# Performance work log

Measured on AMD Instinct MI355X. Metric: run time of the kernel, lower is better.

The kernel has to match this reference:

```python
import jax, jax.numpy as jnp
import numpy as np

B, S, D = 4, 2048, 1024
H = 16
HD = D // H  # 64
BASE = 10000.0


def _rope_cache(seq_len, dim):
    inv_freq = 1.0 / (BASE ** (jnp.arange(0, dim, 2, dtype=jnp.float32) / dim))
    t = jnp.arange(seq_len, dtype=jnp.float32)
    freqs = jnp.einsum('i,j->ij', t, inv_freq)          # [S, dim/2]
    emb = jnp.concatenate([freqs, freqs], axis=-1)      # [S, dim]
    return jnp.cos(emb), jnp.sin(emb)


def _rotate_half(x):
    x1, x2 = jnp.split(x, 2, axis=-1)
    return jnp.concatenate([-x2, x1], axis=-1)


def setup_inputs() -> dict:
    key = jax.random.key(0)
    ks = jax.random.split(key, 5)
    scale = 1.0 / np.sqrt(D)
    return {
        'x': jax.random.normal(ks[0], (B, S, D), dtype=jnp.float32),
        'Wq': jax.random.normal(ks[1], (D, D), dtype=jnp.float32) * scale,
        'Wk': jax.random.normal(ks[2], (D, D), dtype=jnp.float32) * scale,
        'Wv': jax.random.normal(ks[3], (D, D), dtype=jnp.float32) * scale,
        'Wo': jax.random.normal(ks[4], (D, D), dtype=jnp.float32) * scale,
    }


def reference(x, Wq, Wk, Wv, Wo):
    b, s, d = x.shape
    # projections (torch Linear, no bias): y = x @ W.T
    q = (x @ Wq.T).reshape(b, s, H, HD).transpose(0, 2, 1, 3)  # [B,H,S,HD]
    k = (x @ Wk.T).reshape(b, s, H, HD).transpose(0, 2, 1, 3)
    v = (x @ Wv.T).reshape(b, s, H, HD).transpose(0, 2, 1, 3)
    cos, sin = _rope_cache(s, HD)  # [S, HD]
    cos = cos[None, None]
    sin = sin[None, None]
    q = q * cos + _rotate_half(q) * sin
    k = k * cos + _rotate_half(k) * sin
    scale = 1.0 / np.sqrt(HD)
    attn = jnp.einsum('bhqd,bhkd->bhqk', q, k) * scale  # [B,H,S,S]
    attn = jax.nn.softmax(attn, axis=-1)
    out = jnp.einsum('bhqk,bhkd->bhqd', attn, v)
    out = out.transpose(0, 2, 1, 3).reshape(b, s, d)
    return out @ Wo.T
```

## Files before the change

### kernel.cpp

```cpp
#include <hip/hip_runtime.h>
#include <math.h>
#include <stdint.h>

#define BB 4
#define SS 2048
#define DDIM 1024
#define HH 16
#define HD 64
#define QKVLD 3072
#define QSCALE (0.125f * 1.44269504089f)

typedef __bf16 bf16x8 __attribute__((ext_vector_type(8)));
typedef float f32x4 __attribute__((ext_vector_type(4)));
typedef float f32x16 __attribute__((ext_vector_type(16)));
typedef int i32x4 __attribute__((ext_vector_type(4)));

__device__ __forceinline__ unsigned short f2bf(float f) {
    union { float f; unsigned u; } v; v.f = f;
    unsigned r = (v.u + 0x7FFFu + ((v.u >> 16) & 1u)) >> 16;
    return (unsigned short)r;
}
__device__ __forceinline__ void gload_lds16(const unsigned short* g, unsigned char* s) {
    __builtin_amdgcn_global_load_lds(
        (const __attribute__((address_space(1))) unsigned int*)(g),
        (__attribute__((address_space(3))) unsigned int*)(s), 16, 0, 0);
}

__global__ void prep_all(const float* __restrict__ x,
                         const float* __restrict__ Wq, const float* __restrict__ Wk,
                         const float* __restrict__ Wv, const float* __restrict__ Wo,
                         unsigned short* __restrict__ xb,
                         unsigned short* __restrict__ wqkv, unsigned short* __restrict__ wob,
                         float* __restrict__ cosT, float* __restrict__ sinT) {
    int bid = blockIdx.x;
    if (bid < 8192) {
        int i = bid * 256 + threadIdx.x;
        float4 v = ((const float4*)x)[i];
        ushort4 o;
        o.x = f2bf(v.x); o.y = f2bf(v.y); o.z = f2bf(v.z); o.w = f2bf(v.w);
        ((ushort4*)xb)[i] = o;
    } else if (bid < 12288) {
        int i = (bid - 8192) * 256 + threadIdx.x;
        int mat = i >> 18;
        int off = i & 262143;
        const float* src = (mat == 0) ? Wq : (mat == 1) ? Wk : (mat == 2) ? Wv : Wo;
        unsigned short* dst = (mat < 3) ? (wqkv + (size_t)mat * 1048576) : wob;
        float4 v = ((const float4*)src)[off];
        ushort4 o;
        o.x = f2bf(v.x); o.y = f2bf(v.y); o.z = f2bf(v.z); o.w = f2bf(v.w);
        ((ushort4*)dst)[off] = o;
    } else {
        int idx = (bid - 12288) * 256 + threadIdx.x;
        int s = idx >> 5;
        int j = idx & 31;
        float invf = powf(10000.0f, -(float)j / 32.0f);
        float ang = (float)s * invf;
        cosT[idx] = cosf(ang);
        sinT[idx] = sinf(ang);
    }
}

__global__ __launch_bounds__(512) void gemm256_qkv(const unsigned short* __restrict__ A,
                                                   const unsigned short* __restrict__ Bm,
                                                   unsigned short* __restrict__ C,
                                                   const float* __restrict__ cosT,
                                                   const float* __restrict__ sinT,
                                                   unsigned short* __restrict__ vt) {
    __shared__ unsigned char smem[131072];
    const int t = threadIdx.x;
    const int l = t & 63;
    const int w = t >> 6;
    const int wm = w >> 2;
    const int wn = w & 3;
    const int K = DDIM;
    const int NT = K >> 6;

    const int bid = blockIdx.y * gridDim.x + blockIdx.x;
    const int cpx = (gridDim.x * gridDim.y) >> 3;
    const int swz = (bid & 7) * cpx + (bid >> 3);
    const int row0 = (swz / gridDim.x) * 256;
    const int col0 = (swz % gridDim.x) * 256;

    f32x4 acc[8][4];
#pragma unroll
    for (int i = 0; i < 8; ++i)
#pragma unroll
        for (int j = 0; j < 4; ++j) acc[i][j] = f32x4{0.f, 0.f, 0.f, 0.f};

    const unsigned short* aSg = A + (size_t)(row0 + w * 16 + (l >> 3)) * K + ((l & 7) ^ (l >> 3)) * 8;
    const unsigned short* bSg = Bm + (size_t)(col0 + w * 16 + (l >> 3)) * K + ((l & 7) ^ (l >> 3)) * 8;
    const int dRow = (w * 16) * 128;

#define STAGE_A(kt, h, j, buf) \
    gload_lds16(aSg + (size_t)((h) * 128 + (j) * 8) * K + (kt) * 64, \
                smem + (buf) * 65536 + (h) * 16384 + dRow + (j) * 1024)
#define STAGE_B(kt, h, j, buf) \
    gload_lds16(bSg + (size_t)((h) * 128 + (j) * 8) * K + (kt) * 64, \
                smem + (buf) * 65536 + 32768 + (h) * 16384 + dRow + (j) * 1024)

    STAGE_B(0, 0, 0, 0); STAGE_B(0, 0, 1, 0); STAGE_B(0, 1, 0, 0); STAGE_B(0, 1, 1, 0);
    STAGE_A(0, 0, 0, 0); STAGE_A(0, 0, 1, 0); STAGE_A(0, 1, 0, 0); STAGE_A(0, 1, 1, 0);
    STAGE_B(1, 0, 0, 1); STAGE_B(1, 0, 1, 1); STAGE_B(1, 1, 0, 1); STAGE_B(1, 1, 1, 1);
    asm volatile("s_waitcnt vmcnt(4)" ::: "memory");
    __builtin_amdgcn_s_barrier();

    const int cA = (l >> 4) << 4;
    const int swr = (l & 7) << 4;
    const int rA0 = wm * 128 + (l & 15);
    const int rB0 = wn * 64 + (l & 15);

    int cur = 0;
    for (int u = 0; u < NT; ++u) {
        const int nxt = cur ^ 1;
        const unsigned char* Ab = smem + cur * 65536;
        const unsigned char* Bb = smem + cur * 65536 + 32768;
        const bool pA = (u + 1 < NT);
        const bool pB = (u + 2 < NT);
        bf16x8 bfr[4][2];

#pragma unroll
        for (int p = 0; p < 4; ++p) {
            if (p == 0) { if (pA) { STAGE_A(u + 1, 0, 0, nxt); STAGE_A(u + 1, 0, 1, nxt); } }
            if (p == 1) { if (pA) { STAGE_A(u + 1, 1, 0, nxt); STAGE_A(u + 1, 1, 1, nxt); } }
            if (p == 2) { if (pB) { STAGE_B(u + 2, 0, 0, cur); STAGE_B(u + 2, 0, 1, cur); } }
            if (p == 3) { if (pB) { STAGE_B(u + 2, 1, 0, cur); STAGE_B(u + 2, 1, 1, cur); } }

            if (p == 0) {
#pragma unroll
                for (int ni = 0; ni < 4; ++ni)
#pragma unroll
                    for (int kk = 0; kk < 2; ++kk) {
                        int row = rB0 + ni * 16;
                        bfr[ni][kk] = *(const bf16x8*)(Bb + (row * 128 + ((kk * 64 + cA) ^ swr)));
                    }
            }
            bf16x8 af[2][2];
#pragma unroll
            for (int m2 = 0; m2 < 2; ++m2)
#pragma unroll
                for (int kk = 0; kk < 2; ++kk) {
                    int row = rA0 + (p * 2 + m2) * 16;
                    af[m2][kk] = *(const bf16x8*)(Ab + (row * 128 + ((kk * 64 + cA) ^ swr)));
                }

            __builtin_amdgcn_s_barrier();
            asm volatile("s_waitcnt lgkmcnt(0)" ::: "memory");
            __builtin_amdgcn_sched_barrier(0);
            __builtin_amdgcn_s_setprio(1);
#pragma unroll
            for (int m2 = 0; m2 < 2; ++m2)
#pragma unroll
                for (int ni = 0; ni < 4; ++ni)
#pragma unroll
                    for (int kk = 0; kk < 2; ++kk)
                        acc[p * 2 + m2][ni] = __builtin_amdgcn_mfma_f32_16x16x32_bf16(
                            af[m2][kk], bfr[ni][kk], acc[p * 2 + m2][ni], 0, 0, 0);
            __builtin_amdgcn_s_setprio(0);
            if (p == 3) {
                if (u < NT - 2) asm volatile("s_waitcnt vmcnt(4)" ::: "memory");
                else            asm volatile("s_waitcnt vmcnt(0)" ::: "memory");
            }
            __builtin_amdgcn_s_barrier();
        }
        cur = nxt;
    }
#undef STAGE_A
#undef STAGE_B

    const int cr = (l >> 4) << 2;
    const int cc = l & 15;
    const int sec = (col0 + wn * 64) >> 10;

    if (sec == 2) {
#pragma unroll
        for (int mi = 0; mi < 8; ++mi) {
            int s0 = row0 + wm * 128 + mi * 16 + cr;
            int bI = s0 >> 11;
            int sI = s0 & (SS - 1);
#pragma unroll
            for (int ni = 0; ni < 4; ++ni) {
                int vcol = col0 + wn * 64 + ni * 16 + cc - 2048;
                int hh = vcol >> 6, dd = vcol & 63;
                ushort4 o;
                o.x = f2bf(acc[mi][ni][0]);
                o.y = f2bf(acc[mi][ni][1]);
                o.z = f2bf(acc[mi][ni][2]);
                o.w = f2bf(acc[mi][ni][3]);
                *(ushort4*)&vt[((size_t)((bI * HH + hh) * HD + dd)) * SS + sI] = o;
            }
        }
    } else {
        const float qs = (sec == 0) ? QSCALE : 1.0f;
#pragma unroll
        for (int mi = 0; mi < 8; ++mi) {
#pragma unroll
            for (int r = 0; r < 4; ++r) {
                int grow = row0 + wm * 128 + mi * 16 + cr + r;
                int s = grow & (SS - 1);
#pragma unroll
                for (int ni = 0; ni < 2; ++ni) {
                    int j = ni * 16 + cc;
                    float c = cosT[(s << 5) + j];
                    float sn = sinT[(s << 5) + j];
                    float x1 = acc[mi][ni][r], x2 = acc[mi][ni + 2][r];
                    int gcol = col0 + wn * 64 + j;
                    C[(size_t)grow * QKVLD + gcol]      = f2bf((x1 * c - x2 * sn) * qs);
                    C[(size_t)grow * QKVLD + gcol + 32] = f2bf((x2 * c + x1 * sn) * qs);
                }
            }
        }
    }
}

__global__ __launch_bounds__(256) void gemm_bf16_out(const unsigned short* __restrict__ A,
                                                     const unsigned short* __restrict__ Bm,
                                                     float* __restrict__ C,
                                                     int M, int N, int K, int lda) {
    __shared__ unsigned char smem[32768];
    const int t = threadIdx.x;
    const int l = t & 63;
    const int w = t >> 6;
    const int wm = w >> 1, wn = w & 1;

    const int bid = blockIdx.y * gridDim.x + blockIdx.x;
    const int cpx = (gridDim.x * gridDim.y) >> 3;
    const int swz = (bid & 7) * cpx + (bid >> 3);
    const int row0 = (swz / gridDim.x) * 128;
    const int col0 = (swz % gridDim.x) * 128;

    f32x4 acc[4][4];
#pragma unroll
    for (int i = 0; i < 4; ++i)
#pragma unroll
        for (int j = 0; j < 4; ++j) acc[i][j] = f32x4{0.f, 0.f, 0.f, 0.f};

    const int srow = w * 32 + (l >> 2);
    const int scol8 = ((l & 3) ^ ((l >> 3) & 3)) << 3;
    const unsigned short* aS = A + (size_t)(row0 + srow) * lda + scol8;
    const unsigned short* bS = Bm + (size_t)(col0 + srow) * K + scol8;

    int aoff[4], boff[4];
#pragma unroll
    for (int mi = 0; mi < 4; ++mi) {
        int o = (wm * 64 + mi * 16 + (l & 15)) * 64 + ((l >> 4) << 4);
        o ^= ((o >> 7) & 3) << 4;
        aoff[mi] = o;
    }
#pragma unroll
    for (int ni = 0; ni < 4; ++ni) {
        int o = (wn * 64 + ni * 16 + (l & 15)) * 64 + ((l >> 4) << 4);
        o ^= ((o >> 7) & 3) << 4;
        boff[ni] = 8192 + o;
    }

    gload_lds16(aS,                    smem + w * 2048);
    gload_lds16(aS + (size_t)16 * lda, smem + w * 2048 + 1024);
    gload_lds16(bS,                    smem + 8192 + w * 2048);
    gload_lds16(bS + (size_t)16 * K,   smem + 8192 + w * 2048 + 1024);

    int cur = 0;
    for (int k0 = 0; k0 < K; k0 += 32) {
        const int nxt = cur ^ 1;
        if (k0 + 32 < K) {
            const unsigned short* aN = aS + k0 + 32;
            const unsigned short* bN = bS + k0 + 32;
            unsigned char* d = smem + nxt * 16384;
            gload_lds16(aN,                    d + w * 2048);
            gload_lds16(aN + (size_t)16 * lda, d + w * 2048 + 1024);
            gload_lds16(bN,                    d + 8192 + w * 2048);
            gload_lds16(bN + (size_t)16 * K,   d + 8192 + w * 2048 + 1024);
            asm volatile("s_waitcnt vmcnt(4)" ::: "memory");
        } else {
            asm volatile("s_waitcnt vmcnt(0)" ::: "memory");
        }
        __builtin_amdgcn_s_barrier();
        asm volatile("" ::: "memory");

        const unsigned char* base = smem + cur * 16384;
        bf16x8 af[4], bf[4];
#pragma unroll
        for (int mi = 0; mi < 4; ++mi) af[mi] = *(const bf16x8*)(base + aoff[mi]);
#pragma unroll
        for (int ni = 0; ni < 4; ++ni) bf[ni] = *(const bf16x8*)(base + boff[ni]);
#pragma unroll
        for (int mi = 0; mi < 4; ++mi)
#pragma unroll
            for (int ni = 0; ni < 4; ++ni)
                acc[mi][ni] = __builtin_amdgcn_mfma_f32_16x16x32_bf16(af[mi], bf[ni], acc[mi][ni], 0, 0, 0);

        asm volatile("s_waitcnt lgkmcnt(0)" ::: "memory");
        __builtin_amdgcn_s_barrier();
        asm volatile("" ::: "memory");
        cur = nxt;
    }

    const int cr = (l >> 4) << 2;
    const int cc = l & 15;
#pragma unroll
    for (int mi = 0; mi < 4; ++mi)
#pragma unroll
        for (int ni = 0; ni < 4; ++ni) {
            int gcol = col0 + wn * 64 + ni * 16 + cc;
#pragma unroll
            for (int r = 0; r < 4; ++r) {
                int grow = row0 + wm * 64 + mi * 16 + cr + r;
                C[(size_t)grow * N + gcol] = acc[mi][ni][r];
            }
        }
}

__global__ __launch_bounds__(256) void attn_mfma10(const unsigned short* __restrict__ qkv,
                                                   const unsigned short* __restrict__ vt,
                                                   unsigned short* __restrict__ og) {
    __shared__ unsigned char smem[32768];
    const int tid = threadIdx.x;
    const int ln = tid & 63;
    const int w = tid >> 6;
    const int lq = ln & 31;
    const int hi = ln >> 5;

    const int did = blockIdx.x + (blockIdx.y << 4) + (blockIdx.z << 8);
    const int b = did & 3;
    const int h = (did >> 2) & 15;
    const int qb0 = (did >> 6) << 7;

    const int headoff = h * HD;
    const size_t bS = (size_t)b * SS;

    bf16x8 qf[4];
    {
        const unsigned short* qsrc = qkv + (bS + qb0 + w * 32 + lq) * QKVLD + headoff + hi * 8;
#pragma unroll
        for (int dc = 0; dc < 4; ++dc)
            qf[dc] = *(const bf16x8*)(qsrc + dc * 16);
    }

    f32x16 oacc[2];
#pragma unroll
    for (int i = 0; i < 2; ++i)
#pragma unroll
        for (int r = 0; r < 16; ++r) oacc[i][r] = 0.f;
    float lsum = 0.f;

    f32x16 fzero;
#pragma unroll
    for (int r = 0; r < 16; ++r) fzero[r] = 0.f;

    const int srow = w * 16 + (ln >> 3);
    const int scol = ((ln & 7) ^ (ln >> 3)) << 3;
    const unsigned short* kbase_g = qkv + bS * QKVLD + 1024 + headoff;
    const unsigned short* vtbase_g = vt + (size_t)(b * HH + h) * HD * SS;

    {
        const unsigned short* ksrc = kbase_g + (size_t)srow * QKVLD + scol;
        gload_lds16(ksrc,                     smem + w * 2048);
        gload_lds16(ksrc + (size_t)8 * QKVLD, smem + w * 2048 + 1024);
        const unsigned short* vsrc = vtbase_g + (size_t)srow * SS + scol;
        gload_lds16(vsrc,                  smem + 16384 + w * 2048);
        gload_lds16(vsrc + (size_t)8 * SS, smem + 16384 + w * 2048 + 1024);
    }
    __syncthreads();

#pragma unroll 2
    for (int tkv = 0; tkv < SS / 64; ++tkv) {
        const int cur = tkv & 1;
        const int kcur = cur * 8192;
        const int vcur = 16384 + cur * 8192;
        const int nxt = cur ^ 1;
        const bool pre = (tkv + 1 < SS / 64);
        if (pre) {
            const int kv1 = (tkv + 1) * 64;
            const unsigned short* ksrc = kbase_g + (size_t)(kv1 + srow) * QKVLD + scol;
            gload_lds16(ksrc,                     smem + nxt * 8192 + w * 2048);
            gload_lds16(ksrc + (size_t)8 * QKVLD, smem + nxt * 8192 + w * 2048 + 1024);
            const unsigned short* vsrc = vtbase_g + (size_t)srow * SS + kv1 + scol;
            gload_lds16(vsrc,                  smem + 16384 + nxt * 8192 + w * 2048);
            gload_lds16(vsrc + (size_t)8 * SS, smem + 16384 + nxt * 8192 + w * 2048 + 1024);
        }

        f32x16 st[2];
#pragma unroll
        for (int kb = 0; kb < 2; ++kb) {
            bf16x8 kf[4];
#pragma unroll
            for (int dc = 0; dc < 4; ++dc) {
                int row = kb * 32 + lq;
                int o = kcur + ((row * 128 + dc * 32 + hi * 16) ^ ((row & 7) << 4));
                kf[dc] = *(const bf16x8*)(smem + o);
            }
            __builtin_amdgcn_s_setprio(1);
            st[kb] = __builtin_amdgcn_mfma_f32_32x32x16_bf16(kf[0], qf[0], fzero, 0, 0, 0);
#pragma unroll
            for (int dc = 1; dc < 4; ++dc)
                st[kb] = __builtin_amdgcn_mfma_f32_32x32x16_bf16(kf[dc], qf[dc], st[kb], 0, 0, 0);
            __builtin_amdgcn_s_setprio(0);
        }

        float pg[32];
#pragma unroll
        for (int j = 0; j < 16; ++j) pg[j] = __builtin_amdgcn_exp2f(st[0][j]);
#pragma unroll
        for (int j = 0; j < 16; ++j) pg[16 + j] = __builtin_amdgcn_exp2f(st[1][j]);

        i32x4 pwv[4];
#pragma unroll
        for (int g = 0; g < 4; ++g) {
            unsigned u0, u1, u2, u3;
            asm("v_cvt_pk_bf16_f32 %0, %1, %2" : "=v"(u0) : "v"(pg[g * 8 + 0]), "v"(pg[g * 8 + 1]));
            asm("v_cvt_pk_bf16_f32 %0, %1, %2" : "=v"(u1) : "v"(pg[g * 8 + 2]), "v"(pg[g * 8 + 3]));
            asm("v_cvt_pk_bf16_f32 %0, %1, %2" : "=v"(u2) : "v"(pg[g * 8 + 4]), "v"(pg[g * 8 + 5]));
            asm("v_cvt_pk_bf16_f32 %0, %1, %2" : "=v"(u3) : "v"(pg[g * 8 + 6]), "v"(pg[g * 8 + 7]));
            asm("v_permlane32_swap_b32 %0, %1" : "+v"(u0), "+v"(u2));
            asm("v_permlane32_swap_b32 %0, %1" : "+v"(u1), "+v"(u3));
            pwv[g][0] = (int)u0; pwv[g][1] = (int)u1; pwv[g][2] = (int)u2; pwv[g][3] = (int)u3;
        }

        float rs;
        {
            float s0 = (pg[0] + pg[1]) + (pg[2] + pg[3]);
            float s1 = (pg[4] + pg[5]) + (pg[6] + pg[7]);
            float s2 = (pg[8] + pg[9]) + (pg[10] + pg[11]);
            float s3 = (pg[12] + pg[13]) + (pg[14] + pg[15]);
            float s4 = (pg[16] + pg[17]) + (pg[18] + pg[19]);
            float s5 = (pg[20] + pg[21]) + (pg[22] + pg[23]);
            float s6 = (pg[24] + pg[25]) + (pg[26] + pg[27]);
            float s7 = (pg[28] + pg[29]) + (pg[30] + pg[31]);
            rs = ((s0 + s1) + (s2 + s3)) + ((s4 + s5) + (s6 + s7));
        }
        rs += __shfl_xor(rs, 32);
        lsum += rs;

        __builtin_amdgcn_s_setprio(1);
#pragma unroll
        for (int dblk = 0; dblk < 2; ++dblk) {
#pragma unroll
            for (int ks = 0; ks < 4; ++ks) {
                int row = dblk * 32 + lq;
                int o = vcur + ((row * 128 + ks * 32 + hi * 16) ^ ((row & 7) << 4));
                bf16x8 vf = *(const bf16x8*)(smem + o);
                oacc[dblk] = __builtin_amdgcn_mfma_f32_32x32x16_bf16(
                    __builtin_bit_cast(bf16x8, pwv[ks]), vf, oacc[dblk], 0, 0, 0);
            }
        }
        __builtin_amdgcn_s_setprio(0);

        __syncthreads();
    }

    {
        float inv = 1.0f / lsum;
#pragma unroll
        for (int r = 0; r < 16; ++r) {
            int crow = (r & 3) + 8 * (r >> 2) + 4 * hi;
            float invr = __shfl(inv, crow);
            int grow = qb0 + w * 32 + crow;
            size_t base = (bS + grow) * QKVLD + headoff + lq;
            og[base]      = f2bf(oacc[0][r] * invr);
            og[base + 32] = f2bf(oacc[1][r] * invr);
        }
    }
}

extern "C" void kernel_launch(void* const* d_in, const int* in_sizes, int n_in,
                              void* d_out, int out_size, void* d_ws, size_t ws_size,
                              hipStream_t stream) {
    const float* x  = (const float*)d_in[0];
    const float* Wq = (const float*)d_in[1];
    const float* Wk = (const float*)d_in[2];
    const float* Wv = (const float*)d_in[3];
    const float* Wo = (const float*)d_in[4];
    float* out = (float*)d_out;

    const size_t BSD = (size_t)BB * SS * DDIM;
    const size_t WSZ = (size_t)DDIM * DDIM;

    unsigned short* xb   = (unsigned short*)d_ws;
    unsigned short* wqkv = xb + BSD;
    unsigned short* wob  = wqkv + 3 * WSZ;
    unsigned short* qkv  = wob + WSZ;
    unsigned short* vt   = qkv + (size_t)BB * SS * QKVLD;
    float* cosT = (float*)(vt + BSD);
    float* sinT = cosT + (size_t)SS * 32;

    hipLaunchKernelGGL(prep_all, dim3(12544), dim3(256), 0, stream,
                       x, Wq, Wk, Wv, Wo, xb, wqkv, wob, cosT, sinT);

    hipLaunchKernelGGL(gemm256_qkv, dim3(QKVLD / 256, BB * SS / 256), dim3(512), 0, stream,
                       xb, wqkv, qkv, cosT, sinT, vt);

    hipLaunchKernelGGL(attn_mfma10, dim3(SS / 128, HH, BB), dim3(256), 0, stream, qkv, vt, qkv);

    hipLaunchKernelGGL(gemm_bf16_out, dim3(DDIM / 128, BB * SS / 128), dim3(256), 0, stream,
                       qkv, wob, out, BB * SS, DDIM, DDIM, QKVLD);
}
```

Measured before the change: 193.7 us.

## Retile output GEMM to 256x128 pipelined tiles; compute softmax row sums via MFMA

```diff
diff --git a/kernel.cpp b/kernel.cpp
--- a/kernel.cpp
+++ b/kernel.cpp
@@ -212,104 +212,126 @@
     }
 }
 
-__global__ __launch_bounds__(256) void gemm_bf16_out(const unsigned short* __restrict__ A,
-                                                     const unsigned short* __restrict__ Bm,
-                                                     float* __restrict__ C,
-                                                     int M, int N, int K, int lda) {
-    __shared__ unsigned char smem[32768];
+__global__ __launch_bounds__(512) void gemm_out256(const unsigned short* __restrict__ A,
+                                                   const unsigned short* __restrict__ Bm,
+                                                   float* __restrict__ C) {
+    __shared__ unsigned char smem[98304];
     const int t = threadIdx.x;
     const int l = t & 63;
     const int w = t >> 6;
-    const int wm = w >> 1, wn = w & 1;
+    const int wm = w >> 2;
+    const int wn = w & 3;
+    const int K = DDIM;
+    const int NT = K >> 6;
 
     const int bid = blockIdx.y * gridDim.x + blockIdx.x;
     const int cpx = (gridDim.x * gridDim.y) >> 3;
     const int swz = (bid & 7) * cpx + (bid >> 3);
-    const int row0 = (swz / gridDim.x) * 128;
+    const int row0 = (swz / gridDim.x) * 256;
     const int col0 = (swz % gridDim.x) * 128;
 
-    f32x4 acc[4][4];
-#pragma unroll
-    for (int i = 0; i < 4; ++i)
-#pragma unroll
-        for (int j = 0; j < 4; ++j) acc[i][j] = f32x4{0.f, 0.f, 0.f, 0.f};
-
-    const int srow = w * 32 + (l >> 2);
-    const int scol8 = ((l & 3) ^ ((l >> 3) & 3)) << 3;
-    const unsigned short* aS = A + (size_t)(row0 + srow) * lda + scol8;
-    const unsigned short* bS = Bm + (size_t)(col0 + srow) * K + scol8;
-
-    int aoff[4], boff[4];
-#pragma unroll
-    for (int mi = 0; mi < 4; ++mi) {
-        int o = (wm * 64 + mi * 16 + (l & 15)) * 64 + ((l >> 4) << 4);
-        o ^= ((o >> 7) & 3) << 4;
-        aoff[mi] = o;
-    }
-#pragma unroll
-    for (int ni = 0; ni < 4; ++ni) {
-        int o = (wn * 64 + ni * 16 + (l & 15)) * 64 + ((l >> 4) << 4);
-        o ^= ((o >> 7) & 3) << 4;
-        boff[ni] = 8192 + o;
-    }
-
-    gload_lds16(aS,                    smem + w * 2048);
-    gload_lds16(aS + (size_t)16 * lda, smem + w * 2048 + 1024);
-    gload_lds16(bS,                    smem + 8192 + w * 2048);
-    gload_lds16(bS + (size_t)16 * K,   smem + 8192 + w * 2048 + 1024);
+    f32x4 acc[8][2];
+#pragma unroll
+    for (int i = 0; i < 8; ++i)
+#pragma unroll
+        for (int j = 0; j < 2; ++j) acc[i][j] = f32x4{0.f, 0.f, 0.f, 0.f};
+
+    const unsigned short* aSg = A + (size_t)(row0 + w * 8 + (l >> 3)) * QKVLD + ((l & 7) ^ (l >> 3)) * 8;
+    const unsigned short* bSg = Bm + (size_t)(col0 + w * 8 + (l >> 3)) * K + ((l & 7) ^ (l >> 3)) * 8;
+    const int dRow = (w * 8) * 128;
+
+#define SA(kt, c, buf) \
+    gload_lds16(aSg + (size_t)((c) * 64) * QKVLD + (kt) * 64, \
+                smem + (buf) * 49152 + (c) * 8192 + dRow)
+#define SB(kt, c, buf) \
+    gload_lds16(bSg + (size_t)((c) * 64) * K + (kt) * 64, \
+                smem + (buf) * 49152 + 32768 + (c) * 8192 + dRow)
+
+    SB(0, 0, 0); SB(0, 1, 0);
+    SA(0, 0, 0); SA(0, 1, 0); SA(0, 2, 0); SA(0, 3, 0);
+    SB(1, 0, 1); SB(1, 1, 1);
+    asm volatile("s_waitcnt vmcnt(2)" ::: "memory");
+    __builtin_amdgcn_s_barrier();
+
+    const int cA = (l >> 4) << 4;
+    const int swr = (l & 7) << 4;
+    const int rA0 = wm * 128 + (l & 15);
+    const int rB0 = wn * 32 + (l & 15);
 
     int cur = 0;
-    for (int k0 = 0; k0 < K; k0 += 32) {
+    for (int u = 0; u < NT; ++u) {
         const int nxt = cur ^ 1;
-        if (k0 + 32 < K) {
-            const unsigned short* aN = aS + k0 + 32;
-            const unsigned short* bN = bS + k0 + 32;
-            unsigned char* d = smem + nxt * 16384;
-            gload_lds16(aN,                    d + w * 2048);
-            gload_lds16(aN + (size_t)16 * lda, d + w * 2048 + 1024);
-            gload_lds16(bN,                    d + 8192 + w * 2048);
-            gload_lds16(bN + (size_t)16 * K,   d + 8192 + w * 2048 + 1024);
-            asm volatile("s_waitcnt vmcnt(4)" ::: "memory");
-        } else {
-            asm volatile("s_waitcnt vmcnt(0)" ::: "memory");
-        }
-        __builtin_amdgcn_s_barrier();
-        asm volatile("" ::: "memory");
-
-        const unsigned char* base = smem + cur * 16384;
-        bf16x8 af[4], bf[4];
-#pragma unroll
-        for (int mi = 0; mi < 4; ++mi) af[mi] = *(const bf16x8*)(base + aoff[mi]);
-#pragma unroll
-        for (int ni = 0; ni < 4; ++ni) bf[ni] = *(const bf16x8*)(base + boff[ni]);
-#pragma unroll
-        for (int mi = 0; mi < 4; ++mi)
-#pragma unroll
-            for (int ni = 0; ni < 4; ++ni)
-                acc[mi][ni] = __builtin_amdgcn_mfma_f32_16x16x32_bf16(af[mi], bf[ni], acc[mi][ni], 0, 0, 0);
-
-        asm volatile("s_waitcnt lgkmcnt(0)" ::: "memory");
-        __builtin_amdgcn_s_barrier();
-        asm volatile("" ::: "memory");
+        const unsigned char* Ab = smem + cur * 49152;
+        const unsigned char* Bb = smem + cur * 49152 + 32768;
+        const bool pA = (u + 1 < NT);
+        const bool pB = (u + 2 < NT);
+        bf16x8 bfr[2][2];
+
+#pragma unroll
+        for (int p = 0; p < 4; ++p) {
+            if (p == 0) { if (pA) { SA(u + 1, 0, nxt); SA(u + 1, 1, nxt); } }
+            if (p == 1) { if (pA) { SA(u + 1, 2, nxt); SA(u + 1, 3, nxt); } }
+            if (p == 2) { if (pB) { SB(u + 2, 0, cur); } }
+            if (p == 3) { if (pB) { SB(u + 2, 1, cur); } }
+
+            if (p == 0) {
+#pragma unroll
+                for (int ni = 0; ni < 2; ++ni)
+#pragma unroll
+                    for (int kk = 0; kk < 2; ++kk) {
+                        int row = rB0 + ni * 16;
+                        bfr[ni][kk] = *(const bf16x8*)(Bb + (row * 128 + ((kk * 64 + cA) ^ swr)));
+                    }
+            }
+            bf16x8 af[2][2];
+#pragma unroll
+            for (int m2 = 0; m2 < 2; ++m2)
+#pragma unroll
+                for (int kk = 0; kk < 2; ++kk) {
+                    int row = rA0 + (p * 2 + m2) * 16;
+                    af[m2][kk] = *(const bf16x8*)(Ab + (row * 128 + ((kk * 64 + cA) ^ swr)));
+                }
+
+            __builtin_amdgcn_s_barrier();
+            asm volatile("s_waitcnt lgkmcnt(0)" ::: "memory");
+            __builtin_amdgcn_sched_barrier(0);
+            __builtin_amdgcn_s_setprio(1);
+#pragma unroll
+            for (int m2 = 0; m2 < 2; ++m2)
+#pragma unroll
+                for (int ni = 0; ni < 2; ++ni)
+#pragma unroll
+                    for (int kk = 0; kk < 2; ++kk)
+                        acc[p * 2 + m2][ni] = __builtin_amdgcn_mfma_f32_16x16x32_bf16(
+                            af[m2][kk], bfr[ni][kk], acc[p * 2 + m2][ni], 0, 0, 0);
+            __builtin_amdgcn_s_setprio(0);
+            if (p == 3) {
+                if (u < NT - 2) asm volatile("s_waitcnt vmcnt(2)" ::: "memory");
+                else            asm volatile("s_waitcnt vmcnt(0)" ::: "memory");
+            }
+            __builtin_amdgcn_s_barrier();
+        }
         cur = nxt;
     }
+#undef SA
+#undef SB
 
     const int cr = (l >> 4) << 2;
     const int cc = l & 15;
 #pragma unroll
-    for (int mi = 0; mi < 4; ++mi)
-#pragma unroll
-        for (int ni = 0; ni < 4; ++ni) {
-            int gcol = col0 + wn * 64 + ni * 16 + cc;
+    for (int mi = 0; mi < 8; ++mi)
+#pragma unroll
+        for (int ni = 0; ni < 2; ++ni) {
+            int gcol = col0 + wn * 32 + ni * 16 + cc;
 #pragma unroll
             for (int r = 0; r < 4; ++r) {
-                int grow = row0 + wm * 64 + mi * 16 + cr + r;
-                C[(size_t)grow * N + gcol] = acc[mi][ni][r];
-            }
-        }
-}
-
-__global__ __launch_bounds__(256) void attn_mfma10(const unsigned short* __restrict__ qkv,
+                int grow = row0 + wm * 128 + mi * 16 + cr + r;
+                C[(size_t)grow * DDIM + gcol] = acc[mi][ni][r];
+            }
+        }
+}
+
+__global__ __launch_bounds__(256) void attn_mfma11(const unsigned short* __restrict__ qkv,
                                                    const unsigned short* __restrict__ vt,
                                                    unsigned short* __restrict__ og) {
     __shared__ unsigned char smem[32768];
@@ -336,15 +358,21 @@
     }
 
     f32x16 oacc[2];
+    f32x16 lacc;
 #pragma unroll
     for (int i = 0; i < 2; ++i)
 #pragma unroll
         for (int r = 0; r < 16; ++r) oacc[i][r] = 0.f;
-    float lsum = 0.f;
+#pragma unroll
+    for (int r = 0; r < 16; ++r) lacc[r] = 0.f;
 
     f32x16 fzero;
 #pragma unroll
     for (int r = 0; r < 16; ++r) fzero[r] = 0.f;
+
+    i32x4 onesw;
+    onesw[0] = 0x3F803F80; onesw[1] = 0x3F803F80; onesw[2] = 0x3F803F80; onesw[3] = 0x3F803F80;
+    const bf16x8 onesf = __builtin_bit_cast(bf16x8, onesw);
 
     const int srow = w * 16 + (ln >> 3);
     const int scol = ((ln & 7) ^ (ln >> 3)) << 3;
@@ -415,21 +443,6 @@
             pwv[g][0] = (int)u0; pwv[g][1] = (int)u1; pwv[g][2] = (int)u2; pwv[g][3] = (int)u3;
         }
 
-        float rs;
-        {
-            float s0 = (pg[0] + pg[1]) + (pg[2] + pg[3]);
-            float s1 = (pg[4] + pg[5]) + (pg[6] + pg[7]);
-            float s2 = (pg[8] + pg[9]) + (pg[10] + pg[11]);
-            float s3 = (pg[12] + pg[13]) + (pg[14] + pg[15]);
-            float s4 = (pg[16] + pg[17]) + (pg[18] + pg[19]);
-            float s5 = (pg[20] + pg[21]) + (pg[22] + pg[23]);
-            float s6 = (pg[24] + pg[25]) + (pg[26] + pg[27]);
-            float s7 = (pg[28] + pg[29]) + (pg[30] + pg[31]);
-            rs = ((s0 + s1) + (s2 + s3)) + ((s4 + s5) + (s6 + s7));
-        }
-        rs += __shfl_xor(rs, 32);
-        lsum += rs;
-
         __builtin_amdgcn_s_setprio(1);
 #pragma unroll
         for (int dblk = 0; dblk < 2; ++dblk) {
@@ -442,22 +455,23 @@
                     __builtin_bit_cast(bf16x8, pwv[ks]), vf, oacc[dblk], 0, 0, 0);
             }
         }
+#pragma unroll
+        for (int ks = 0; ks < 4; ++ks)
+            lacc = __builtin_amdgcn_mfma_f32_32x32x16_bf16(
+                __builtin_bit_cast(bf16x8, pwv[ks]), onesf, lacc, 0, 0, 0);
         __builtin_amdgcn_s_setprio(0);
 
         __syncthreads();
     }
 
-    {
-        float inv = 1.0f / lsum;
-#pragma unroll
-        for (int r = 0; r < 16; ++r) {
-            int crow = (r & 3) + 8 * (r >> 2) + 4 * hi;
-            float invr = __shfl(inv, crow);
-            int grow = qb0 + w * 32 + crow;
-            size_t base = (bS + grow) * QKVLD + headoff + lq;
-            og[base]      = f2bf(oacc[0][r] * invr);
-            og[base + 32] = f2bf(oacc[1][r] * invr);
-        }
+#pragma unroll
+    for (int r = 0; r < 16; ++r) {
+        int crow = (r & 3) + 8 * (r >> 2) + 4 * hi;
+        float invr = 1.0f / lacc[r];
+        int grow = qb0 + w * 32 + crow;
+        size_t base = (bS + grow) * QKVLD + headoff + lq;
+        og[base]      = f2bf(oacc[0][r] * invr);
+        og[base + 32] = f2bf(oacc[1][r] * invr);
     }
 }
 
@@ -488,8 +502,8 @@
     hipLaunchKernelGGL(gemm256_qkv, dim3(QKVLD / 256, BB * SS / 256), dim3(512), 0, stream,
                        xb, wqkv, qkv, cosT, sinT, vt);
 
-    hipLaunchKernelGGL(attn_mfma10, dim3(SS / 128, HH, BB), dim3(256), 0, stream, qkv, vt, qkv);
-
-    hipLaunchKernelGGL(gemm_bf16_out, dim3(DDIM / 128, BB * SS / 128), dim3(256), 0, stream,
-                       qkv, wob, out, BB * SS, DDIM, DDIM, QKVLD);
-}
+    hipLaunchKernelGGL(attn_mfma11, dim3(SS / 128, HH, BB), dim3(256), 0, stream, qkv, vt, qkv);
+
+    hipLaunchKernelGGL(gemm_out256, dim3(DDIM / 128, BB * SS / 256), dim3(512), 0, stream,
+                       qkv, wob, out);
+}
```

New measurement: 193.2 us. No clear change (-0.3%).
